# Performance work log

Measured on AMD Instinct MI355X. Metric: run time of the kernel, lower is better.

## Reference

```python
import jax, jax.numpy as jnp
import numpy as np

EMBED_DIM = 1024
NUM_HEADS = 16
HEAD_DIM = EMBED_DIM // NUM_HEADS
SCALE = HEAD_DIM ** -0.5


def setup_inputs() -> dict:
    key = jax.random.key(0)
    k_x, k_qkv_w, k_qkv_b, k_p_w, k_p_b = jax.random.split(key, 5)
    B, N, C = 4, 2048, EMBED_DIM
    std = C ** -0.5
    return {
        "x": jax.random.normal(k_x, (B, N, C), dtype=jnp.float32),
        "qkv_w": jax.random.normal(k_qkv_w, (C, 3 * C), dtype=jnp.float32) * std,
        "qkv_b": jax.random.normal(k_qkv_b, (3 * C,), dtype=jnp.float32) * 0.02,
        "proj_w": jax.random.normal(k_p_w, (C, C), dtype=jnp.float32) * std,
        "proj_b": jax.random.normal(k_p_b, (C,), dtype=jnp.float32) * 0.02,
    }


def reference(x, qkv_w, qkv_b, proj_w, proj_b):
    B, N, C = x.shape
    H, D = NUM_HEADS, HEAD_DIM
    # fused QKV projection: [B, N, 3C] -> [3, B, H, N, D]
    qkv = (x @ qkv_w + qkv_b).reshape(B, N, 3, H, D).transpose(2, 0, 3, 1, 4)
    q, k, v = qkv[0], qkv[1], qkv[2]
    # explicit N x N attention (faithful to the original, no fused SDPA)
    attn = jnp.einsum("bhqd,bhkd->bhqk", q, k) * SCALE
    attn = jax.nn.softmax(attn, axis=-1)
    out = jnp.einsum("bhqk,bhkd->bhqd", attn, v)  # [B, H, N, D]
    out = out.transpose(0, 2, 1, 3).reshape(B, N, C)
    return out @ proj_w + proj_b
```

## Files before the change

kernel.cpp:

```cpp
#include <hip/hip_runtime.h>
#include <hip/hip_bf16.h>

typedef __bf16 bf16x8 __attribute__((ext_vector_type(8)));
typedef __bf16 bf16x4 __attribute__((ext_vector_type(4)));
typedef float  f32x4  __attribute__((ext_vector_type(4)));

#define MFMA_BF16(a, b, c) __builtin_amdgcn_mfma_f32_16x16x32_bf16((a), (b), (c), 0, 0, 0)

typedef const __attribute__((address_space(1))) void* gas_ptr;
typedef __attribute__((address_space(3))) void* las_ptr;

__device__ __forceinline__ void gload_lds16(const void* g, void* l) {
    __builtin_amdgcn_global_load_lds((gas_ptr)g, (las_ptr)l, 16, 0, 0);
}

#define LOG2E 1.44269504088896f
#define QSCALE 0.1803368801111204f

__global__ __launch_bounds__(256) void cvt_f32_bf16(const float* __restrict__ in,
                                                    __bf16* __restrict__ out, int n4) {
    int i = blockIdx.x * 256 + threadIdx.x;
    if (i < n4) {
        float4 v = ((const float4*)in)[i];
        bf16x4 o = {(__bf16)v.x, (__bf16)v.y, (__bf16)v.z, (__bf16)v.w};
        ((bf16x4*)out)[i] = o;
    }
}

__global__ __launch_bounds__(256) void transpose_cvt(const float* __restrict__ in,
                                                     __bf16* __restrict__ out, int R, int C) {
    __shared__ float t[32][33];
    int bx = blockIdx.x * 32, by = blockIdx.y * 32;
    int x = bx + threadIdx.x;
    for (int j = threadIdx.y; j < 32; j += 8)
        t[j][threadIdx.x] = in[(size_t)(by + j) * C + x];
    __syncthreads();
    int x2 = by + threadIdx.x;
    for (int j = threadIdx.y; j < 32; j += 8)
        out[(size_t)(bx + j) * R + x2] = (__bf16)t[threadIdx.x][j];
}

template <int MODE>
__global__ __launch_bounds__(256) void gemm_bt(const __bf16* __restrict__ A,
                                               const __bf16* __restrict__ Bt,
                                               const float* __restrict__ bias,
                                               float* __restrict__ outp,
                                               __bf16* __restrict__ Qp,
                                               __bf16* __restrict__ Kp,
                                               __bf16* __restrict__ Vp,
                                               int M, int Nn, int K) {
    __shared__ __align__(16) __bf16 As[128 * 32];
    __shared__ __align__(16) __bf16 Bs[128 * 32];
    const int tid = threadIdx.x, lane = tid & 63, w = tid >> 6;
    const int wr = w >> 1, wc = w & 1;
    const int row0 = blockIdx.y * 128, col0 = blockIdx.x * 128;
    const __bf16* Ag = A + (size_t)row0 * K;
    const __bf16* Bg = Bt + (size_t)col0 * K;
    const int lr = lane >> 2;
    const int lk = (lane & 3) * 8;
    const int frow = lane & 15, fq = lane >> 4;
    f32x4 acc[4][4];
    for (int i = 0; i < 4; ++i)
        for (int j = 0; j < 4; ++j) acc[i][j] = (f32x4)0.f;

    for (int k0 = 0; k0 < K; k0 += 32) {
        __syncthreads();
        for (int it = 0; it < 2; ++it) {
            int ci = 2 * w + it;
            gload_lds16(Ag + (size_t)(ci * 16 + lr) * K + k0 + lk, &As[ci * 512]);
            gload_lds16(Bg + (size_t)(ci * 16 + lr) * K + k0 + lk, &Bs[ci * 512]);
        }
        __syncthreads();
        bf16x8 af[4], bf[4];
        for (int i = 0; i < 4; ++i)
            af[i] = *(const bf16x8*)&As[(wr * 64 + i * 16 + frow) * 32 + fq * 8];
        for (int j = 0; j < 4; ++j)
            bf[j] = *(const bf16x8*)&Bs[(wc * 64 + j * 16 + frow) * 32 + fq * 8];
        for (int i = 0; i < 4; ++i)
            for (int j = 0; j < 4; ++j) acc[i][j] = MFMA_BF16(af[i], bf[j], acc[i][j]);
    }

    for (int i = 0; i < 4; ++i) {
        int rbase = row0 + wr * 64 + i * 16 + fq * 4;
        for (int j = 0; j < 4; ++j) {
            int c = col0 + wc * 64 + j * 16 + frow;
            float bv = bias[c];
            if (MODE == 0) {
                int which = c >> 10;
                int h = (c >> 6) & 15;
                int d = c & 63;
                if (which == 2) {
                    int b = rbase >> 11, n = rbase & 2047;
                    bf16x4 vv = {(__bf16)(acc[i][j][0] + bv), (__bf16)(acc[i][j][1] + bv),
                                 (__bf16)(acc[i][j][2] + bv), (__bf16)(acc[i][j][3] + bv)};
                    *(bf16x4*)&Vp[(size_t)(((b << 4) + h) * 64 + d) * 2048 + n] = vv;
                } else {
                    for (int rg = 0; rg < 4; ++rg) {
                        int rr = rbase + rg;
                        int b = rr >> 11, n = rr & 2047;
                        float v = acc[i][j][rg] + bv;
                        if (which == 0)
                            Qp[(size_t)(((b << 4) + h) * 2048 + n) * 64 + d] =
                                (__bf16)(v * QSCALE);
                        else
                            Kp[(size_t)(((b << 4) + h) * 2048 + n) * 64 + d] = (__bf16)v;
                    }
                }
            } else {
                for (int rg = 0; rg < 4; ++rg)
                    outp[(size_t)(rbase + rg) * Nn + c] = acc[i][j][rg] + bv;
            }
        }
    }
}

__global__ __launch_bounds__(256, 4) void flash_attn4(const __bf16* __restrict__ Q,
                                                      const __bf16* __restrict__ K,
                                                      const __bf16* __restrict__ Vt,
                                                      __bf16* __restrict__ O) {
    __shared__ __align__(16) __bf16 Kts[2][4096];
    __shared__ __align__(16) __bf16 Vts[2][4096];
    __shared__ __align__(16) __bf16 Ps[4][1024];
    const int tid = threadIdx.x, lane = tid & 63, w = tid >> 6;
    const int frow = lane & 15, fq = lane >> 4;
    const int bh = blockIdx.y;
    const int q0 = blockIdx.x * 128;
    const __bf16* Qg = Q + ((size_t)bh * 2048 + q0 + w * 32) * 64;
    const __bf16* Kb = K + (size_t)bh * 2048 * 64;
    const __bf16* Vb = Vt + (size_t)bh * 64 * 2048;

    bf16x8 qf[2][2];
#pragma unroll
    for (int nt = 0; nt < 2; ++nt)
#pragma unroll
        for (int ks = 0; ks < 2; ++ks)
            qf[nt][ks] = *(const bf16x8*)(Qg + (nt * 16 + frow) * 64 + ks * 32 + fq * 8);

    bf16x8 ones;
#pragma unroll
    for (int i = 0; i < 8; ++i) ones[i] = (__bf16)1.0f;

    f32x4 acc[2][4];
#pragma unroll
    for (int i = 0; i < 2; ++i)
#pragma unroll
        for (int j = 0; j < 4; ++j) acc[i][j] = (f32x4)0.f;
    f32x4 acc_l[2];
#pragma unroll
    for (int i = 0; i < 2; ++i) acc_l[i] = (f32x4)0.f;

    const int s_r16 = lane >> 2;
    const int s_c8 = (lane & 3) * 8;

    auto stage = [&](int kt, int buf) {
#pragma unroll
        for (int it = 0; it < 2; ++it) {
            int ci = 2 * w + it;
            int ks = ci >> 2;
            int r16 = (ci & 3) * 16 + s_r16;
            gload_lds16(Kb + (size_t)(kt * 64 + r16) * 64 + ks * 32 + s_c8,
                        &Kts[buf][ci * 512]);
            gload_lds16(Vb + (size_t)r16 * 2048 + kt * 64 + ks * 32 + s_c8,
                        &Vts[buf][ci * 512]);
        }
    };

    stage(0, 0);

    const int swz = frow & 3;
    const int pe = (fq ^ swz) * 8;
    __bf16* Pw = Ps[w];

    for (int kt = 0; kt < 32; ++kt) {
        const int cur = kt & 1;
        __syncthreads();
        if (kt < 31) stage(kt + 1, cur ^ 1);

        const __bf16* Kc = Kts[cur];
        const __bf16* Vc = Vts[cur];

#pragma unroll
        for (int ph = 0; ph < 2; ++ph) {
#pragma unroll
            for (int mi = 0; mi < 2; ++mi) {
                int mt = ph * 2 + mi;
                bf16x8 a0 = *(const bf16x8*)&Kc[(mt * 16 + frow) * 32 + fq * 8];
                bf16x8 a1 = *(const bf16x8*)&Kc[2048 + (mt * 16 + frow) * 32 + fq * 8];
                f32x4 s[2];
#pragma unroll
                for (int nt = 0; nt < 2; ++nt) {
                    s[nt] = MFMA_BF16(a0, qf[nt][0], (f32x4)0.f);
                    s[nt] = MFMA_BF16(a1, qf[nt][1], s[nt]);
                }
                int u = mi * 2 + (fq >> 1);
                int e = ((u ^ swz) << 3) + ((fq & 1) << 2);
#pragma unroll
                for (int nt = 0; nt < 2; ++nt) {
                    float p0 = __builtin_exp2f(s[nt][0]);
                    float p1 = __builtin_exp2f(s[nt][1]);
                    float p2 = __builtin_exp2f(s[nt][2]);
                    float p3 = __builtin_exp2f(s[nt][3]);
                    bf16x4 pk = {(__bf16)p0, (__bf16)p1, (__bf16)p2, (__bf16)p3};
                    *(bf16x4*)&Pw[(nt * 16 + frow) * 32 + e] = pk;
                }
            }

            bf16x8 vf[4];
#pragma unroll
            for (int nt = 0; nt < 4; ++nt)
                vf[nt] = *(const bf16x8*)&Vc[ph * 2048 + (nt * 16 + frow) * 32 + fq * 8];
#pragma unroll
            for (int mq = 0; mq < 2; ++mq) {
                bf16x8 p = *(const bf16x8*)&Pw[(mq * 16 + frow) * 32 + pe];
#pragma unroll
                for (int nt = 0; nt < 4; ++nt)
                    acc[mq][nt] = MFMA_BF16(p, vf[nt], acc[mq][nt]);
                acc_l[mq] = MFMA_BF16(p, ones, acc_l[mq]);
            }
        }
    }

    const int b = bh >> 4, h = bh & 15;
#pragma unroll
    for (int mq = 0; mq < 2; ++mq)
#pragma unroll
        for (int r = 0; r < 4; ++r) {
            float linv = 1.0f / acc_l[mq][r];
            int qg = q0 + w * 32 + mq * 16 + fq * 4 + r;
            __bf16* orow = O + ((size_t)(b * 2048 + qg)) * 1024 + h * 64 + frow;
#pragma unroll
            for (int nt = 0; nt < 4; ++nt)
                orow[nt * 16] = (__bf16)(acc[mq][nt][r] * linv);
        }
}

extern "C" void kernel_launch(void* const* d_in, const int* in_sizes, int n_in,
                              void* d_out, int out_size, void* d_ws, size_t ws_size,
                              hipStream_t stream) {
    const float* x      = (const float*)d_in[0];
    const float* qkv_w  = (const float*)d_in[1];
    const float* qkv_b  = (const float*)d_in[2];
    const float* proj_w = (const float*)d_in[3];
    const float* proj_b = (const float*)d_in[4];
    float* out = (float*)d_out;

    char* ws = (char*)d_ws;
    __bf16* Xb     = (__bf16*)(ws);
    __bf16* Wqkvt  = (__bf16*)(ws + 16777216);
    __bf16* Wpt    = (__bf16*)(ws + 23068672);
    __bf16* Qb     = (__bf16*)(ws + 25165824);
    __bf16* Kb     = (__bf16*)(ws + 41943040);
    __bf16* Vtb    = (__bf16*)(ws + 58720256);
    __bf16* AttnOut = Xb;

    cvt_f32_bf16<<<8192, 256, 0, stream>>>(x, Xb, 2097152);
    transpose_cvt<<<dim3(96, 32), dim3(32, 8), 0, stream>>>(qkv_w, Wqkvt, 1024, 3072);
    transpose_cvt<<<dim3(32, 32), dim3(32, 8), 0, stream>>>(proj_w, Wpt, 1024, 1024);

    gemm_bt<0><<<dim3(24, 64), 256, 0, stream>>>(Xb, Wqkvt, qkv_b, nullptr,
                                                 Qb, Kb, Vtb, 8192, 3072, 1024);

    flash_attn4<<<dim3(16, 64), 256, 0, stream>>>(Qb, Kb, Vtb, AttnOut);

    gemm_bt<1><<<dim3(8, 64), 256, 0, stream>>>(AttnOut, Wpt, proj_b, out,
                                                nullptr, nullptr, nullptr, 8192, 1024, 1024);
}
```

Measured before the change: 315.3 us.

## Keep softmax probabilities in registers and swizzle K/V LDS tiles

```diff
diff --git a/kernel.cpp b/kernel.cpp
--- a/kernel.cpp
+++ b/kernel.cpp
@@ -114,13 +114,12 @@
     }
 }
 
-__global__ __launch_bounds__(256, 4) void flash_attn4(const __bf16* __restrict__ Q,
+__global__ __launch_bounds__(256, 4) void flash_attn5(const __bf16* __restrict__ Q,
                                                       const __bf16* __restrict__ K,
                                                       const __bf16* __restrict__ Vt,
                                                       __bf16* __restrict__ O) {
     __shared__ __align__(16) __bf16 Kts[2][4096];
     __shared__ __align__(16) __bf16 Vts[2][4096];
-    __shared__ __align__(16) __bf16 Ps[4][1024];
     const int tid = threadIdx.x, lane = tid & 63, w = tid >> 6;
     const int frow = lane & 15, fq = lane >> 4;
     const int bh = blockIdx.y;
@@ -150,7 +149,7 @@
     for (int i = 0; i < 2; ++i) acc_l[i] = (f32x4)0.f;
 
     const int s_r16 = lane >> 2;
-    const int s_c8 = (lane & 3) * 8;
+    const int s_c8 = (((lane & 3) ^ ((lane >> 3) & 3))) * 8;
 
     auto stage = [&](int kt, int buf) {
 #pragma unroll
@@ -167,9 +166,10 @@
 
     stage(0, 0);
 
-    const int swz = frow & 3;
-    const int pe = (fq ^ swz) * 8;
-    __bf16* Pw = Ps[w];
+    const int key = (frow >> 1) & 3;
+    const int kslot = (fq ^ key) * 8;
+    const int vA = (((fq >> 1) ^ key)) * 8 + (fq & 1) * 4;
+    const int vB = ((((fq >> 1) | 2) ^ key)) * 8 + (fq & 1) * 4;
 
     for (int kt = 0; kt < 32; ++kt) {
         const int cur = kt & 1;
@@ -181,42 +181,38 @@
 
 #pragma unroll
         for (int ph = 0; ph < 2; ++ph) {
+            bf16x8 pf[2];
 #pragma unroll
             for (int mi = 0; mi < 2; ++mi) {
                 int mt = ph * 2 + mi;
-                bf16x8 a0 = *(const bf16x8*)&Kc[(mt * 16 + frow) * 32 + fq * 8];
-                bf16x8 a1 = *(const bf16x8*)&Kc[2048 + (mt * 16 + frow) * 32 + fq * 8];
-                f32x4 s[2];
+                bf16x8 a0 = *(const bf16x8*)&Kc[(mt * 16 + frow) * 32 + kslot];
+                bf16x8 a1 = *(const bf16x8*)&Kc[2048 + (mt * 16 + frow) * 32 + kslot];
 #pragma unroll
                 for (int nt = 0; nt < 2; ++nt) {
-                    s[nt] = MFMA_BF16(a0, qf[nt][0], (f32x4)0.f);
-                    s[nt] = MFMA_BF16(a1, qf[nt][1], s[nt]);
-                }
-                int u = mi * 2 + (fq >> 1);
-                int e = ((u ^ swz) << 3) + ((fq & 1) << 2);
-#pragma unroll
-                for (int nt = 0; nt < 2; ++nt) {
-                    float p0 = __builtin_exp2f(s[nt][0]);
-                    float p1 = __builtin_exp2f(s[nt][1]);
-                    float p2 = __builtin_exp2f(s[nt][2]);
-                    float p3 = __builtin_exp2f(s[nt][3]);
-                    bf16x4 pk = {(__bf16)p0, (__bf16)p1, (__bf16)p2, (__bf16)p3};
-                    *(bf16x4*)&Pw[(nt * 16 + frow) * 32 + e] = pk;
+                    f32x4 s = MFMA_BF16(a0, qf[nt][0], (f32x4)0.f);
+                    s = MFMA_BF16(a1, qf[nt][1], s);
+                    pf[nt][mi * 4 + 0] = (__bf16)__builtin_exp2f(s[0]);
+                    pf[nt][mi * 4 + 1] = (__bf16)__builtin_exp2f(s[1]);
+                    pf[nt][mi * 4 + 2] = (__bf16)__builtin_exp2f(s[2]);
+                    pf[nt][mi * 4 + 3] = (__bf16)__builtin_exp2f(s[3]);
                 }
             }
 
-            bf16x8 vf[4];
-#pragma unroll
-            for (int nt = 0; nt < 4; ++nt)
-                vf[nt] = *(const bf16x8*)&Vc[ph * 2048 + (nt * 16 + frow) * 32 + fq * 8];
-#pragma unroll
-            for (int mq = 0; mq < 2; ++mq) {
-                bf16x8 p = *(const bf16x8*)&Pw[(mq * 16 + frow) * 32 + pe];
-#pragma unroll
-                for (int nt = 0; nt < 4; ++nt)
-                    acc[mq][nt] = MFMA_BF16(p, vf[nt], acc[mq][nt]);
-                acc_l[mq] = MFMA_BF16(p, ones, acc_l[mq]);
+#pragma unroll
+            for (int nt = 0; nt < 4; ++nt) {
+                const __bf16* vrow = &Vc[ph * 2048 + (nt * 16 + frow) * 32];
+                bf16x4 lo = *(const bf16x4*)&vrow[vA];
+                bf16x4 hi = *(const bf16x4*)&vrow[vB];
+                bf16x8 vf;
+                vf[0] = lo[0]; vf[1] = lo[1]; vf[2] = lo[2]; vf[3] = lo[3];
+                vf[4] = hi[0]; vf[5] = hi[1]; vf[6] = hi[2]; vf[7] = hi[3];
+#pragma unroll
+                for (int mq = 0; mq < 2; ++mq)
+                    acc[mq][nt] = MFMA_BF16(pf[mq], vf, acc[mq][nt]);
             }
+#pragma unroll
+            for (int mq = 0; mq < 2; ++mq)
+                acc_l[mq] = MFMA_BF16(pf[mq], ones, acc_l[mq]);
         }
     }
 
@@ -260,7 +256,7 @@
     gemm_bt<0><<<dim3(24, 64), 256, 0, stream>>>(Xb, Wqkvt, qkv_b, nullptr,
                                                  Qb, Kb, Vtb, 8192, 3072, 1024);
 
-    flash_attn4<<<dim3(16, 64), 256, 0, stream>>>(Qb, Kb, Vtb, AttnOut);
+    flash_attn5<<<dim3(16, 64), 256, 0, stream>>>(Qb, Kb, Vtb, AttnOut);
 
     gemm_bt<1><<<dim3(8, 64), 256, 0, stream>>>(AttnOut, Wpt, proj_b, out,
                                                 nullptr, nullptr, nullptr, 8192, 1024, 1024);
```

Result: no change. 313.0 us (-0.7%).
